# Optimization experiments

Hardware: AMD Instinct MI355X
Metric: run time of the kernel (lower is better)

Reference implementation:

```python
import jax, jax.numpy as jnp
import numpy as np

H, D, VD = 8, 64, 64
QD, KD, VDIM, OUT = 512, 512, 512, 512
N, QS, VS = 16, 512, 512
TEMP = 10.0              # softstair_temp
SCALING = D ** -0.5


def _softstair(x):
    fl = jnp.floor(x)
    return fl + jax.nn.sigmoid(TEMP * (jnp.abs(x - fl) - 0.5))


def setup_inputs() -> dict:
    key = jax.random.key(0)
    ks = jax.random.split(key, 24)
    f = jax.random.normal
    s = 0.03  # xavier-ish scale
    return {
        "Q": f(ks[0], (N, QS, QD), jnp.float32),
        "K": f(ks[1], (N, VS, KD), jnp.float32),
        "V": f(ks[2], (N, VS, VDIM), jnp.float32),
        "past_state": f(ks[3], (N, H, QS, D), jnp.float32),
        "past_attention": jax.random.uniform(ks[4], (N, H, QS, 1), jnp.float32),
        "value_positions": jnp.arange(VS, dtype=jnp.float32),
        "attention_mask": jnp.ones((N, QS, VS), jnp.int32),
        "Wq": f(ks[5], (QD, H * D), jnp.float32) * s,
        "Wk": f(ks[6], (KD, H * D), jnp.float32) * s,
        "Wv": f(ks[7], (VDIM, H * VD), jnp.float32) * s,
        "Wpos": f(ks[8], (QD, H * D), jnp.float32) * s,
        "bpos": f(ks[9], (H * D,), jnp.float32) * s,
        "Wsigma": f(ks[10], (H, D, 1), jnp.float32) * s,
        "Wrho": f(ks[11], (H, D, 3), jnp.float32) * s,
        "mix_w": f(ks[12], (QD, 1), jnp.float32) * s,
        "mix_b": f(ks[13], (1,), jnp.float32) * s,
        "gru_wi": f(ks[14], (D, 3 * D), jnp.float32) * s,
        "gru_wh": f(ks[15], (D, 3 * D), jnp.float32) * s,
        "gru_bi": f(ks[16], (3 * D,), jnp.float32) * s,
        "gru_bh": f(ks[17], (3 * D,), jnp.float32) * s,
        "Wc": f(ks[18], (H * VD, OUT), jnp.float32) * s,
    }


def reference(Q, K, V, past_state, past_attention, value_positions, attention_mask,
              Wq, Wk, Wv, Wpos, bpos, Wsigma, Wrho, mix_w, mix_b,
              gru_wi, gru_wh, gru_bi, gru_bh, Wc):
    n, qS, _ = Q.shape
    vS = K.shape[1]
    mask_f = attention_mask.astype(jnp.float32)          # [N,qS,vS]
    mask_b = attention_mask.astype(bool)[:, None]        # [N,1,qS,vS]
    lengths = jnp.sum(mask_f, axis=-1)                   # [N,qS]
    l_1 = jnp.maximum(1.0, lengths - 1.0)[:, None, :, None]
    step_size = 1.0 / l_1                                # [N,1,qS,1]
    nvp = value_positions[None, None, None, :] * step_size  # [N,1,qS,vS]

    # mix gate
    mix = jax.nn.sigmoid(Q @ mix_w + mix_b)[:, None]     # [N,1,qS,1]

    # projections -> [N,H,S,d]
    Qpos = (Q @ Wpos + bpos).reshape(n, qS, H, D).transpose(0, 2, 1, 3)
    Qh = (Q @ Wq).reshape(n, qS, H, D).transpose(0, 2, 1, 3)
    Kh = (K @ Wk).reshape(n, vS, H, D).transpose(0, 2, 1, 3)
    Vh = (V @ Wv).reshape(n, vS, H, VD).transpose(0, 2, 1, 3)

    # content attention
    content = jnp.einsum('bhqd,bhkd->bhqk', Qh, Kh) * SCALING
    content_attn = jax.nn.softmax(jnp.where(mask_b, content, -jnp.inf), axis=-1)

    # GRUCell update (torch gate order r,z,n) on relu(Qpos) with past_state
    x = jax.nn.relu(Qpos)
    gi = x @ gru_wi + gru_bi
    gh = past_state @ gru_wh + gru_bh
    ir, iz, inn = jnp.split(gi, 3, axis=-1)
    hr, hz, hn = jnp.split(gh, 3, axis=-1)
    r = jax.nn.sigmoid(ir + hr)
    z = jax.nn.sigmoid(iz + hz)
    nn_ = jnp.tanh(inn + r * hn)
    state = (1.0 - z) * nn_ + z * past_state             # [N,H,qS,D]

    # location (Gaussian) attention
    sigma = (jax.nn.relu(jnp.einsum('bhqd,hde->bhqe', state, Wsigma)) + 0.27) \
            / lengths[:, None, :, None]                  # [N,H,qS,1]
    rho = jnp.einsum('bhqd,hde->bhqe', state, Wrho)      # [N,H,qS,3]
    steps = _softstair(rho[..., 0:1])
    attn_gate = jax.nn.sigmoid(rho[..., 1:2])
    bias_gate = jax.nn.sigmoid(rho[..., 2:3])
    mu_ = steps * step_size + attn_gate * past_attention + bias_gate
    # leaky clamp to [0,1]
    mu = jnp.maximum(0.01 * mu_, jnp.minimum(mu_, 1.0 + 0.01 * mu_))
    diff = nvp - mu                                      # [N,H,qS,vS]
    gauss = jnp.exp(-(diff * diff) / (2.0 * sigma * sigma))
    g = gauss * mask_f[:, None]
    pos_attn = g / jnp.sum(g + 1e-20, axis=-1, keepdims=True)

    scores = mix * pos_attn + (1.0 - mix) * content_attn
    attended = jnp.einsum('bhqk,bhkv->bhqv', scores, Vh)
    out = attended.transpose(0, 2, 1, 3).reshape(n, qS, H * VD) @ Wc
    return out
```

## Files before the change

### kernel.cpp

```cpp
#include <hip/hip_runtime.h>


typedef __bf16 bf16;
typedef __bf16 bfx8 __attribute__((ext_vector_type(8)));
typedef float v4f __attribute__((ext_vector_type(4)));

__device__ inline float sigm(float x) { return 1.0f / (1.0f + __expf(-x)); }
__device__ inline float tanh_fast(float x) { return 1.0f - 2.0f / (__expf(2.0f * x) + 1.0f); }

__device__ inline v4f mfma16(bfx8 a, bfx8 b, v4f c) {
    return __builtin_amdgcn_mfma_f32_16x16x32_bf16(a, b, c, 0, 0, 0);
}

__device__ inline void split8(const float* __restrict__ p, bfx8& hi, bfx8& lo) {
    float4 x = *(const float4*)p;
    float4 y = *(const float4*)(p + 4);
    float v[8] = {x.x, x.y, x.z, x.w, y.x, y.y, y.z, y.w};
#pragma unroll
    for (int j = 0; j < 8; ++j) {
        bf16 h = (bf16)v[j];
        hi[j] = h;
        lo[j] = (bf16)(v[j] - (float)h);
    }
}

__device__ inline bfx8 cvt8(const float* __restrict__ p) {
    float4 x = *(const float4*)p;
    float4 y = *(const float4*)(p + 4);
    bfx8 o;
    o[0] = (bf16)x.x; o[1] = (bf16)x.y; o[2] = (bf16)x.z; o[3] = (bf16)x.w;
    o[4] = (bf16)y.x; o[5] = (bf16)y.y; o[6] = (bf16)y.z; o[7] = (bf16)y.w;
    return o;
}

__device__ inline unsigned short bfbits(float v) {
    bf16 h = (bf16)v;
    return __builtin_bit_cast(unsigned short, h);
}
__device__ inline float bffrom(unsigned short u) {
    return (float)__builtin_bit_cast(bf16, u);
}

struct TW { const float* src[5]; bf16* dst[5]; bf16* dstlo[5]; };

__global__ __launch_bounds__(256) void trans_w_kernel(TW a) {
    __shared__ float tile[64][68];
    const float* src = a.src[blockIdx.y];
    bf16* dst = a.dst[blockIdx.y];
    bf16* dlo = a.dstlo[blockIdx.y];
    const int rbase = (blockIdx.x >> 3) * 64, cbase = (blockIdx.x & 7) * 64;
    const int t = threadIdx.x;
    const int r = t >> 2, cc = (t & 3) * 16;
    {
        const float* p = src + (long)(rbase + r) * 512 + cbase + cc;
        *(float4*)(&tile[r][cc]) = *(const float4*)p;
        *(float4*)(&tile[r][cc + 4]) = *(const float4*)(p + 4);
        *(float4*)(&tile[r][cc + 8]) = *(const float4*)(p + 8);
        *(float4*)(&tile[r][cc + 12]) = *(const float4*)(p + 12);
    }
    __syncthreads();
    {
        bfx8 h0, h1, l0, l1;
#pragma unroll
        for (int j = 0; j < 8; ++j) {
            float v0 = tile[cc + j][r];
            float v1 = tile[cc + 8 + j][r];
            bf16 a0 = (bf16)v0, a1 = (bf16)v1;
            h0[j] = a0; l0[j] = (bf16)(v0 - (float)a0);
            h1[j] = a1; l1[j] = (bf16)(v1 - (float)a1);
        }
        bf16* p = dst + (long)(cbase + r) * 512 + rbase + cc;
        *(bfx8*)p = h0;
        *(bfx8*)(p + 8) = h1;
        if (dlo) {
            bf16* pl = dlo + (long)(cbase + r) * 512 + rbase + cc;
            *(bfx8*)pl = l0;
            *(bfx8*)(pl + 8) = l1;
        }
    }
}

__global__ void gru_prep_kernel(const float* __restrict__ gwi, const float* __restrict__ gwh,
                                bf16* ih, bf16* il, bf16* hh, bf16* hl) {
    const float* src = blockIdx.x ? gwh : gwi;
    bf16* dh = blockIdx.x ? hh : ih;
    bf16* dl = blockIdx.x ? hl : il;
    int n = threadIdx.x;
    for (int k = 0; k < 64; ++k) {
        float v = src[k * 192 + n];
        bf16 h = (bf16)v;
        dh[n * 64 + k] = h;
        dl[n * 64 + k] = (bf16)(v - (float)h);
    }
}

struct G3 { const float* A[3]; const bf16* BT[3]; bf16* C[3]; };

__global__ __launch_bounds__(256) void gemm_bt3(G3 g) {
    __shared__ bf16 As[64][72];
    __shared__ bf16 Bs[64][72];

    const int z = blockIdx.z;
    const float* __restrict__ A = g.A[z];
    const bf16* __restrict__ BT = g.BT[z];
    bf16* __restrict__ C = g.C[z];

    const int mbase = blockIdx.x * 64, nbase = blockIdx.y * 64;
    const int t = threadIdx.x;
    const int wave = t >> 6, lane = t & 63;
    const int quad = lane >> 4, c = lane & 15;
    const int wrow = (wave >> 1) * 32, wcol = (wave & 1) * 32;

    const v4f zero4 = {0.f, 0.f, 0.f, 0.f};
    v4f acc[2][2];
    acc[0][0] = zero4; acc[0][1] = zero4; acc[1][0] = zero4; acc[1][1] = zero4;

    const int sr = t >> 2, sch = t & 3;

    for (int k0 = 0; k0 < 512; k0 += 32) {
        bfx8 va = cvt8(A + (long)(mbase + sr) * 512 + k0 + sch * 8);
        bfx8 vb = *(const bfx8*)(BT + (long)(nbase + sr) * 512 + k0 + sch * 8);
        *(bfx8*)(&As[sr][sch * 8]) = va;
        *(bfx8*)(&Bs[sr][sch * 8]) = vb;
        __syncthreads();

        bfx8 a0 = *(const bfx8*)(&As[wrow + c][quad * 8]);
        bfx8 a1 = *(const bfx8*)(&As[wrow + 16 + c][quad * 8]);
        bfx8 b0 = *(const bfx8*)(&Bs[wcol + c][quad * 8]);
        bfx8 b1 = *(const bfx8*)(&Bs[wcol + 16 + c][quad * 8]);
        acc[0][0] = mfma16(a0, b0, acc[0][0]);
        acc[0][1] = mfma16(a0, b1, acc[0][1]);
        acc[1][0] = mfma16(a1, b0, acc[1][0]);
        acc[1][1] = mfma16(a1, b1, acc[1][1]);
        __syncthreads();
    }

    if (z == 2) {
#pragma unroll
        for (int tm = 0; tm < 2; ++tm)
#pragma unroll
            for (int tn = 0; tn < 2; ++tn)
#pragma unroll
                for (int i = 0; i < 4; ++i) {
                    int rl = wrow + tm * 16 + quad * 4 + i;
                    int cl = wcol + tn * 16 + c;
                    As[cl][rl] = (bf16)acc[tm][tn][i];
                }
        __syncthreads();
        bf16* CT = C + ((long)(mbase >> 9)) * 262144 + (long)nbase * 512 + (mbase & 511);
        const int rr = t >> 2, kc = (t & 3) * 16;
        bfx8 o0, o1;
#pragma unroll
        for (int j = 0; j < 8; ++j) { o0[j] = As[rr][kc + j]; o1[j] = As[rr][kc + 8 + j]; }
        *(bfx8*)(CT + (long)rr * 512 + kc) = o0;
        *(bfx8*)(CT + (long)rr * 512 + kc + 8) = o1;
    } else {
#pragma unroll
        for (int tm = 0; tm < 2; ++tm)
#pragma unroll
            for (int tn = 0; tn < 2; ++tn)
#pragma unroll
                for (int i = 0; i < 4; ++i) {
                    int row = mbase + wrow + tm * 16 + quad * 4 + i;
                    int col = nbase + wcol + tn * 16 + c;
                    C[(long)row * 512 + col] = (bf16)acc[tm][tn][i];
                }
    }
}

__global__ __launch_bounds__(256) void gemm_out(
    const bf16* __restrict__ A, const bf16* __restrict__ BT, float* __restrict__ C) {
    __shared__ bf16 As[64][72];
    __shared__ bf16 Bs[64][72];

    const int mbase = blockIdx.x * 64, nbase = blockIdx.y * 64;
    const int t = threadIdx.x;
    const int wave = t >> 6, lane = t & 63;
    const int quad = lane >> 4, c = lane & 15;
    const int wrow = (wave >> 1) * 32, wcol = (wave & 1) * 32;

    const v4f zero4 = {0.f, 0.f, 0.f, 0.f};
    v4f acc[2][2];
    acc[0][0] = zero4; acc[0][1] = zero4; acc[1][0] = zero4; acc[1][1] = zero4;

    const int sr = t >> 2, sch = t & 3;

    for (int k0 = 0; k0 < 512; k0 += 32) {
        bfx8 va = *(const bfx8*)(A + (long)(mbase + sr) * 512 + k0 + sch * 8);
        bfx8 vb = *(const bfx8*)(BT + (long)(nbase + sr) * 512 + k0 + sch * 8);
        *(bfx8*)(&As[sr][sch * 8]) = va;
        *(bfx8*)(&Bs[sr][sch * 8]) = vb;
        __syncthreads();

        bfx8 a0 = *(const bfx8*)(&As[wrow + c][quad * 8]);
        bfx8 a1 = *(const bfx8*)(&As[wrow + 16 + c][quad * 8]);
        bfx8 b0 = *(const bfx8*)(&Bs[wcol + c][quad * 8]);
        bfx8 b1 = *(const bfx8*)(&Bs[wcol + 16 + c][quad * 8]);
        acc[0][0] = mfma16(a0, b0, acc[0][0]);
        acc[0][1] = mfma16(a0, b1, acc[0][1]);
        acc[1][0] = mfma16(a1, b0, acc[1][0]);
        acc[1][1] = mfma16(a1, b1, acc[1][1]);
        __syncthreads();
    }

#pragma unroll
    for (int tm = 0; tm < 2; ++tm)
#pragma unroll
        for (int tn = 0; tn < 2; ++tn)
#pragma unroll
            for (int i = 0; i < 4; ++i) {
                int row = mbase + wrow + tm * 16 + quad * 4 + i;
                int col = nbase + wcol + tn * 16 + c;
                C[(long)row * 512 + col] = acc[tm][tn][i];
            }
}

__global__ __launch_bounds__(256) void gemm_split_hl(
    const float* __restrict__ A, const bf16* __restrict__ BTh,
    const bf16* __restrict__ BTl, const float* __restrict__ bias,
    bf16* __restrict__ Ch, bf16* __restrict__ Cl) {
    __shared__ bf16 Ah[64][72], Al[64][72];
    __shared__ bf16 Bh[64][72], Bl[64][72];

    const int mbase = blockIdx.x * 64, nbase = blockIdx.y * 64;
    const int t = threadIdx.x;
    const int wave = t >> 6, lane = t & 63;
    const int quad = lane >> 4, c = lane & 15;
    const int wrow = (wave >> 1) * 32, wcol = (wave & 1) * 32;

    const v4f zero4 = {0.f, 0.f, 0.f, 0.f};
    v4f acc[2][2];
    acc[0][0] = zero4; acc[0][1] = zero4; acc[1][0] = zero4; acc[1][1] = zero4;

    const int sr = t >> 2, sch = t & 3;

    for (int k0 = 0; k0 < 512; k0 += 32) {
        bfx8 h, l;
        split8(A + (long)(mbase + sr) * 512 + k0 + sch * 8, h, l);
        *(bfx8*)(&Ah[sr][sch * 8]) = h;
        *(bfx8*)(&Al[sr][sch * 8]) = l;
        *(bfx8*)(&Bh[sr][sch * 8]) = *(const bfx8*)(BTh + (long)(nbase + sr) * 512 + k0 + sch * 8);
        *(bfx8*)(&Bl[sr][sch * 8]) = *(const bfx8*)(BTl + (long)(nbase + sr) * 512 + k0 + sch * 8);
        __syncthreads();

        bfx8 ah0 = *(const bfx8*)(&Ah[wrow + c][quad * 8]);
        bfx8 ah1 = *(const bfx8*)(&Ah[wrow + 16 + c][quad * 8]);
        bfx8 al0 = *(const bfx8*)(&Al[wrow + c][quad * 8]);
        bfx8 al1 = *(const bfx8*)(&Al[wrow + 16 + c][quad * 8]);
        bfx8 bh0 = *(const bfx8*)(&Bh[wcol + c][quad * 8]);
        bfx8 bh1 = *(const bfx8*)(&Bh[wcol + 16 + c][quad * 8]);
        bfx8 bl0 = *(const bfx8*)(&Bl[wcol + c][quad * 8]);
        bfx8 bl1 = *(const bfx8*)(&Bl[wcol + 16 + c][quad * 8]);
        acc[0][0] = mfma16(ah0, bh0, acc[0][0]);
        acc[0][0] = mfma16(ah0, bl0, acc[0][0]);
        acc[0][0] = mfma16(al0, bh0, acc[0][0]);
        acc[0][1] = mfma16(ah0, bh1, acc[0][1]);
        acc[0][1] = mfma16(ah0, bl1, acc[0][1]);
        acc[0][1] = mfma16(al0, bh1, acc[0][1]);
        acc[1][0] = mfma16(ah1, bh0, acc[1][0]);
        acc[1][0] = mfma16(ah1, bl0, acc[1][0]);
        acc[1][0] = mfma16(al1, bh0, acc[1][0]);
        acc[1][1] = mfma16(ah1, bh1, acc[1][1]);
        acc[1][1] = mfma16(ah1, bl1, acc[1][1]);
        acc[1][1] = mfma16(al1, bh1, acc[1][1]);
        __syncthreads();
    }

#pragma unroll
    for (int tm = 0; tm < 2; ++tm)
#pragma unroll
        for (int tn = 0; tn < 2; ++tn)
#pragma unroll
            for (int i = 0; i < 4; ++i) {
                int row = mbase + wrow + tm * 16 + quad * 4 + i;
                int col = nbase + wcol + tn * 16 + c;
                float v = fmaxf(acc[tm][tn][i] + bias[col], 0.f);
                bf16 h = (bf16)v;
                Ch[(long)row * 512 + col] = h;
                Cl[(long)row * 512 + col] = (bf16)(v - (float)h);
            }
}

__global__ __launch_bounds__(256) void mix_len_kernel(
    const float* __restrict__ Q, const int* __restrict__ mask,
    const float* __restrict__ mix_w, const float* __restrict__ mix_b,
    float* __restrict__ mixv, float* __restrict__ stepv, float* __restrict__ lenv,
    unsigned* __restrict__ maskbits) {
    int row = blockIdx.x * 4 + (threadIdx.x >> 6);
    int lane = threadIdx.x & 63;
    float dot = 0.f, ms = 0.f;
    unsigned myw = 0;
#pragma unroll
    for (int j = 0; j < 8; ++j) {
        float qv = Q[(long)row * 512 + j * 64 + lane];
        float wv = mix_w[j * 64 + lane];
        dot += qv * wv;
        int mv = mask[(long)row * 512 + j * 64 + lane];
        unsigned long long b = __ballot(mv != 0);
        ms += (float)__popcll(b);
        if ((lane >> 1) == j) myw = (unsigned)(b >> ((lane & 1) * 32));
    }
#pragma unroll
    for (int o = 32; o > 0; o >>= 1) dot += __shfl_xor(dot, o);
    if (lane < 16) maskbits[(long)row * 16 + lane] = myw;
    if (lane == 0) {
        mixv[row] = sigm(dot + mix_b[0]);
        lenv[row] = ms;
        stepv[row] = 1.0f / fmaxf(1.0f, ms - 1.0f);
    }
}

__global__ __launch_bounds__(256) void gru_fused_kernel(
    const bf16* __restrict__ Xh, const bf16* __restrict__ Xl,
    const float* __restrict__ hp,
    const bf16* __restrict__ wih, const bf16* __restrict__ wil,
    const bf16* __restrict__ whh, const bf16* __restrict__ whl,
    const float* __restrict__ gbi, const float* __restrict__ gbh,
    const float* __restrict__ pa, const float* __restrict__ Wsigma,
    const float* __restrict__ Wrho,
    const float* __restrict__ lenv, const float* __restrict__ stepv,
    float* __restrict__ muv, float* __restrict__ sigv) {
    __shared__ bf16 Wh[192][72], Wl[192][72];
    __shared__ float biL[384];

    const int b = blockIdx.x;
    const int qb = b & 7, nh = b >> 3, hd = nh & 7, n = nh >> 3;
    const int t = threadIdx.x;
    const int w = t >> 6, lane = t & 63, quad = lane >> 4, c = lane & 15;
    const int q0 = qb * 64 + w * 16;

    if (t < 192) { biL[t] = gbi[t]; biL[192 + t] = gbh[t]; }
#pragma unroll
    for (int it = 0; it < 6; ++it) {
        int task = it * 256 + t;
        int r = task >> 3, ch = task & 7;
        *(bfx8*)(&Wh[r][ch * 8]) = *(const bfx8*)(wih + r * 64 + ch * 8);
        *(bfx8*)(&Wl[r][ch * 8]) = *(const bfx8*)(wil + r * 64 + ch * 8);
    }
    __syncthreads();

    const v4f zero4 = {0.f, 0.f, 0.f, 0.f};
    v4f gi[12], gh[12];
#pragma unroll
    for (int nt = 0; nt < 12; ++nt) gi[nt] = zero4;
#pragma unroll
    for (int ks = 0; ks < 2; ++ks) {
        long ao = (long)(n * 512 + q0 + c) * 512 + hd * 64 + ks * 32 + quad * 8;
        bfx8 xh = *(const bfx8*)(Xh + ao);
        bfx8 xl = *(const bfx8*)(Xl + ao);
#pragma unroll
        for (int nt = 0; nt < 12; ++nt) {
            bfx8 bh = *(const bfx8*)(&Wh[nt * 16 + c][ks * 32 + quad * 8]);
            bfx8 bl = *(const bfx8*)(&Wl[nt * 16 + c][ks * 32 + quad * 8]);
            gi[nt] = mfma16(xh, bh, gi[nt]);
            gi[nt] = mfma16(xh, bl, gi[nt]);
            gi[nt] = mfma16(xl, bh, gi[nt]);
        }
    }
    __syncthreads();
#pragma unroll
    for (int it = 0; it < 6; ++it) {
        int task = it * 256 + t;
        int r = task >> 3, ch = task & 7;
        *(bfx8*)(&Wh[r][ch * 8]) = *(const bfx8*)(whh + r * 64 + ch * 8);
        *(bfx8*)(&Wl[r][ch * 8]) = *(const bfx8*)(whl + r * 64 + ch * 8);
    }
    __syncthreads();
#pragma unroll
    for (int nt = 0; nt < 12; ++nt) gh[nt] = zero4;
#pragma unroll
    for (int ks = 0; ks < 2; ++ks) {
        bfx8 ah, al;
        split8(hp + (long)(nh * 512 + q0 + c) * 64 + ks * 32 + quad * 8, ah, al);
#pragma unroll
        for (int nt = 0; nt < 12; ++nt) {
            bfx8 bh = *(const bfx8*)(&Wh[nt * 16 + c][ks * 32 + quad * 8]);
            bfx8 bl = *(const bfx8*)(&Wl[nt * 16 + c][ks * 32 + quad * 8]);
            gh[nt] = mfma16(ah, bh, gh[nt]);
            gh[nt] = mfma16(ah, bl, gh[nt]);
            gh[nt] = mfma16(al, bh, gh[nt]);
        }
    }

    float st[4][4];
#pragma unroll
    for (int t4 = 0; t4 < 4; ++t4) {
        float bir = biL[t4 * 16 + c];
        float biz = biL[64 + t4 * 16 + c];
        float bin = biL[128 + t4 * 16 + c];
        float bhr = biL[192 + t4 * 16 + c];
        float bhz = biL[256 + t4 * 16 + c];
        float bhn = biL[320 + t4 * 16 + c];
#pragma unroll
        for (int i = 0; i < 4; ++i) {
            int row = q0 + quad * 4 + i;
            float r = sigm(gi[t4][i] + bir + gh[t4][i] + bhr);
            float z = sigm(gi[t4 + 4][i] + biz + gh[t4 + 4][i] + bhz);
            float nn_ = tanh_fast(gi[t4 + 8][i] + bin + r * (gh[t4 + 8][i] + bhn));
            float hpv = hp[(long)(nh * 512 + row) * 64 + t4 * 16 + c];
            st[t4][i] = (1.0f - z) * nn_ + z * hpv;
        }
    }

    float ws_[4], wr0[4], wr1[4], wr2[4];
#pragma unroll
    for (int t4 = 0; t4 < 4; ++t4) {
        int d = t4 * 16 + c;
        ws_[t4] = Wsigma[hd * 64 + d];
        wr0[t4] = Wrho[(hd * 64 + d) * 3 + 0];
        wr1[t4] = Wrho[(hd * 64 + d) * 3 + 1];
        wr2[t4] = Wrho[(hd * 64 + d) * 3 + 2];
    }
#pragma unroll
    for (int i = 0; i < 4; ++i) {
        float s0 = 0.f, s1 = 0.f, s2 = 0.f, s3 = 0.f;
#pragma unroll
        for (int t4 = 0; t4 < 4; ++t4) {
            float sv = st[t4][i];
            s0 += sv * ws_[t4];
            s1 += sv * wr0[t4];
            s2 += sv * wr1[t4];
            s3 += sv * wr2[t4];
        }
#pragma unroll
        for (int o = 1; o < 16; o <<= 1) {
            s0 += __shfl_xor(s0, o);
            s1 += __shfl_xor(s1, o);
            s2 += __shfl_xor(s2, o);
            s3 += __shfl_xor(s3, o);
        }
        if (c == 0) {
            int row = q0 + quad * 4 + i;
            int idx = nh * 512 + row, rq = n * 512 + row;
            float L = lenv[rq], sp = stepv[rq];
            float sg = (fmaxf(s0, 0.f) + 0.27f) / L;
            float fl = floorf(s1);
            float steps = fl + sigm(10.0f * (fabsf(s1 - fl) - 0.5f));
            float ag = sigm(s2), bg = sigm(s3);
            float mu_ = steps * sp + ag * pa[idx] + bg;
            float mu = fmaxf(0.01f * mu_, fminf(mu_, 1.0f + 0.01f * mu_));
            muv[idx] = mu;
            sigv[idx] = sg;
        }
    }
}

__global__ __launch_bounds__(256) void attn_fused_kernel(
    const bf16* __restrict__ Qh, const bf16* __restrict__ Kh,
    const bf16* __restrict__ VhT, const unsigned* __restrict__ maskbits,
    const float* __restrict__ vpos, const float* __restrict__ mixv,
    const float* __restrict__ stepv, const float* __restrict__ muv,
    const float* __restrict__ sigv, bf16* __restrict__ att) {
    __shared__ bf16 Plds[16][520];
    __shared__ float vps[512];
    __shared__ unsigned mb[16][16];
    __shared__ float rmax[4][16], rsum[4][16], rgsum[4][16];
    __shared__ float rowmu[16], rowsig[16], rowstep[16], rowmix[16];

    const int b = blockIdx.x;
    const int nh = ((b >> 8) << 3) | (b & 7);
    const int qt = (b >> 3) & 31;
    const int hd = nh & 7, n = nh >> 3;
    const int t = threadIdx.x;

    if (t < 16) {
        int q = qt * 16 + t;
        int idx = nh * 512 + q, rq = n * 512 + q;
        rowmu[t] = muv[idx];
        rowsig[t] = sigv[idx];
        rowstep[t] = stepv[rq];
        rowmix[t] = mixv[rq];
    }
    vps[t] = vpos[t];
    vps[256 + t] = vpos[256 + t];
    mb[t >> 4][t & 15] = maskbits[(long)(n * 512 + qt * 16 + (t >> 4)) * 16 + (t & 15)];

    const int wave = t >> 6, lane = t & 63;
    const int quad = lane >> 4, c = lane & 15;
    const int qloc = quad * 4;

    const bf16* qrow = Qh + (long)(n * 512 + qt * 16 + c) * 512 + hd * 64 + quad * 8;
    bfx8 afr0 = *(const bfx8*)qrow;
    bfx8 afr1 = *(const bfx8*)(qrow + 32);

    const v4f zero4 = {0.f, 0.f, 0.f, 0.f};
    v4f acc[8];
#pragma unroll
    for (int i = 0; i < 8; ++i) acc[i] = zero4;

    const bf16* kbase = Kh + (long)(n * 512 + wave * 128 + c) * 512 + hd * 64 + quad * 8;
#pragma unroll
    for (int t8 = 0; t8 < 8; ++t8) {
        bfx8 b0 = *(const bfx8*)(kbase + (long)t8 * 16 * 512);
        bfx8 b1 = *(const bfx8*)(kbase + (long)t8 * 16 * 512 + 32);
        acc[t8] = mfma16(afr0, b0, acc[t8]);
        acc[t8] = mfma16(afr1, b1, acc[t8]);
    }
#pragma unroll
    for (int t8 = 0; t8 < 8; ++t8) acc[t8] = acc[t8] * 0.125f;

    __syncthreads();

    unsigned mbits[4] = {0u, 0u, 0u, 0u};
#pragma unroll
    for (int t8 = 0; t8 < 8; ++t8) {
        int wd = wave * 4 + (t8 >> 1);
        int bit = (t8 & 1) * 16 + c;
#pragma unroll
        for (int i = 0; i < 4; ++i)
            mbits[i] |= ((mb[qloc + i][wd] >> bit) & 1u) << t8;
    }

#pragma unroll
    for (int i = 0; i < 4; ++i) {
        float mx = -3.0e38f;
#pragma unroll
        for (int t8 = 0; t8 < 8; ++t8)
            if ((mbits[i] >> t8) & 1u) mx = fmaxf(mx, acc[t8][i]);
        mx = fmaxf(mx, __shfl_xor(mx, 1));
        mx = fmaxf(mx, __shfl_xor(mx, 2));
        mx = fmaxf(mx, __shfl_xor(mx, 4));
        mx = fmaxf(mx, __shfl_xor(mx, 8));
        if (c == 0) rmax[wave][qloc + i] = mx;
    }
    __syncthreads();

    float gmx[4], inv2s[4];
#pragma unroll
    for (int i = 0; i < 4; ++i) {
        gmx[i] = fmaxf(fmaxf(rmax[0][qloc + i], rmax[1][qloc + i]),
                       fmaxf(rmax[2][qloc + i], rmax[3][qloc + i]));
        float sg = rowsig[qloc + i];
        inv2s[i] = 0.5f / (sg * sg);
    }

    float psum[4] = {0.f, 0.f, 0.f, 0.f};
    float gsum[4] = {0.f, 0.f, 0.f, 0.f};
    unsigned pg[8][4];
#pragma unroll
    for (int t8 = 0; t8 < 8; ++t8) {
        int k = wave * 128 + t8 * 16 + c;
        float vp = vps[k];
#pragma unroll
        for (int i = 0; i < 4; ++i) {
            int on = (mbits[i] >> t8) & 1;
            float pv = on ? __expf(acc[t8][i] - gmx[i]) : 0.f;
            float d = vp * rowstep[qloc + i] - rowmu[qloc + i];
            float gv = on ? __expf(-(d * d) * inv2s[i]) : 0.f;
            psum[i] += pv;
            gsum[i] += gv;
            pg[t8][i] = ((unsigned)bfbits(gv) << 16) | (unsigned)bfbits(pv);
        }
    }
#pragma unroll
    for (int i = 0; i < 4; ++i) {
#pragma unroll
        for (int o = 1; o < 16; o <<= 1) {
            psum[i] += __shfl_xor(psum[i], o);
            gsum[i] += __shfl_xor(gsum[i], o);
        }
        if (c == 0) {
            rsum[wave][qloc + i] = psum[i];
            rgsum[wave][qloc + i] = gsum[i];
        }
    }
    __syncthreads();

    float ac[4], bc[4];
#pragma unroll
    for (int i = 0; i < 4; ++i) {
        float Sp = rsum[0][qloc + i] + rsum[1][qloc + i] + rsum[2][qloc + i] + rsum[3][qloc + i];
        float Sg = rgsum[0][qloc + i] + rgsum[1][qloc + i] + rgsum[2][qloc + i] +
                   rgsum[3][qloc + i] + 512.0f * 1e-20f;
        float m_ = rowmix[qloc + i];
        ac[i] = (1.0f - m_) / Sp;
        bc[i] = m_ / Sg;
    }

#pragma unroll
    for (int t8 = 0; t8 < 8; ++t8) {
        int k = wave * 128 + t8 * 16 + c;
#pragma unroll
        for (int i = 0; i < 4; ++i) {
            float pv = bffrom((unsigned short)(pg[t8][i] & 0xffffu));
            float gv = bffrom((unsigned short)(pg[t8][i] >> 16));
            Plds[qloc + i][k] = (bf16)(pv * ac[i] + gv * bc[i]);
        }
    }
    __syncthreads();

    v4f accO = zero4;
    const bf16* vrow = VhT + (long)(n * 512 + hd * 64 + wave * 16 + c) * 512 + quad * 8;
#pragma unroll
    for (int ks = 0; ks < 16; ++ks) {
        bfx8 af = *(const bfx8*)(&Plds[c][ks * 32 + quad * 8]);
        bfx8 bf_ = *(const bfx8*)(vrow + ks * 32);
        accO = mfma16(af, bf_, accO);
    }

#pragma unroll
    for (int i = 0; i < 4; ++i) {
        att[(long)(n * 512 + qt * 16 + quad * 4 + i) * 512 + hd * 64 + wave * 16 + c] =
            (bf16)accO[i];
    }
}

extern "C" void kernel_launch(void* const* d_in, const int* in_sizes, int n_in,
                              void* d_out, int out_size, void* d_ws, size_t ws_size,
                              hipStream_t stream) {
    (void)in_sizes; (void)n_in; (void)out_size; (void)ws_size;

    const float* Q = (const float*)d_in[0];
    const float* K = (const float*)d_in[1];
    const float* V = (const float*)d_in[2];
    const float* past_state = (const float*)d_in[3];
    const float* past_att = (const float*)d_in[4];
    const float* vpos = (const float*)d_in[5];
    const int* mask = (const int*)d_in[6];
    const float* Wq = (const float*)d_in[7];
    const float* Wk = (const float*)d_in[8];
    const float* Wv = (const float*)d_in[9];
    const float* Wpos = (const float*)d_in[10];
    const float* bpos = (const float*)d_in[11];
    const float* Wsigma = (const float*)d_in[12];
    const float* Wrho = (const float*)d_in[13];
    const float* mix_w = (const float*)d_in[14];
    const float* mix_b = (const float*)d_in[15];
    const float* gwi = (const float*)d_in[16];
    const float* gwh = (const float*)d_in[17];
    const float* gbi = (const float*)d_in[18];
    const float* gbh = (const float*)d_in[19];
    const float* Wc = (const float*)d_in[20];
    float* out = (float*)d_out;

    char* p = (char*)d_ws;
    const size_t SZB = 8192UL * 512 * 2;
    const size_t SZW = 512UL * 512 * 2;
    bf16* WqT = (bf16*)p;   p += SZW;
    bf16* WkT = (bf16*)p;   p += SZW;
    bf16* WvT = (bf16*)p;   p += SZW;
    bf16* WpT = (bf16*)p;   p += SZW;
    bf16* WpTl = (bf16*)p;  p += SZW;
    bf16* WcT = (bf16*)p;   p += SZW;
    bf16* wih = (bf16*)p;   p += 24576;
    bf16* wil = (bf16*)p;   p += 24576;
    bf16* whh = (bf16*)p;   p += 24576;
    bf16* whl = (bf16*)p;   p += 24576;
    bf16* Qh = (bf16*)p;    p += SZB;
    bf16* Kh = (bf16*)p;    p += SZB;
    bf16* VhT = (bf16*)p;   p += SZB;
    bf16* Xh = (bf16*)p;
    bf16* att = Xh;         p += SZB;
    bf16* Xl = (bf16*)p;    p += SZB;
    unsigned* maskbits = (unsigned*)p;   p += 8192UL * 16 * 4;
    float* mixv = (float*)p;  p += 32768;
    float* stepv = (float*)p; p += 32768;
    float* lenv = (float*)p;  p += 32768;
    float* muv = (float*)p;   p += 262144;
    float* sigv = (float*)p;  p += 262144;

    dim3 blk(256);
    dim3 gProj(128, 8, 1);

    TW tw;
    tw.src[0] = Wq; tw.src[1] = Wk; tw.src[2] = Wv; tw.src[3] = Wpos; tw.src[4] = Wc;
    tw.dst[0] = WqT; tw.dst[1] = WkT; tw.dst[2] = WvT; tw.dst[3] = WpT; tw.dst[4] = WcT;
    tw.dstlo[0] = nullptr; tw.dstlo[1] = nullptr; tw.dstlo[2] = nullptr;
    tw.dstlo[3] = WpTl; tw.dstlo[4] = nullptr;
    trans_w_kernel<<<dim3(64, 5), blk, 0, stream>>>(tw);

    gru_prep_kernel<<<dim3(2), dim3(192), 0, stream>>>(gwi, gwh, wih, wil, whh, whl);

    G3 g;
    g.A[0] = Q; g.A[1] = K; g.A[2] = V;
    g.BT[0] = WqT; g.BT[1] = WkT; g.BT[2] = WvT;
    g.C[0] = Qh; g.C[1] = Kh; g.C[2] = VhT;
    gemm_bt3<<<dim3(128, 8, 3), blk, 0, stream>>>(g);

    gemm_split_hl<<<gProj, blk, 0, stream>>>(Q, WpT, WpTl, bpos, Xh, Xl);

    mix_len_kernel<<<dim3(2048), blk, 0, stream>>>(Q, mask, mix_w, mix_b, mixv, stepv, lenv, maskbits);

    gru_fused_kernel<<<dim3(1024), blk, 0, stream>>>(
        Xh, Xl, past_state, wih, wil, whh, whl, gbi, gbh, past_att, Wsigma, Wrho,
        lenv, stepv, muv, sigv);

    attn_fused_kernel<<<dim3(4096), blk, 0, stream>>>(
        Qh, Kh, VhT, maskbits, vpos, mixv, stepv, muv, sigv, att);

    gemm_out<<<gProj, blk, 0, stream>>>(att, WcT, out);
}
```

Before: 361.3 us.

## Drop softmax max pass, split P/G matmuls, defer normalization to output

The attention kernel now skips the row-max reduction and its barrier and exponentiates scaled scores directly. This relies on the scores being small enough not to overflow. It writes unnormalized content and positional weights to two LDS tiles and runs two MFMA accumulations against V. Both normalizations and the mix are applied to the final accumulators, which removes one barrier and the per-element rescale pass, at the cost of doubling the P·V MFMA work and LDS reads. Per-row parameters, mask bits and value positions are now read straight from global memory instead of being staged in shared memory.

```diff
diff --git a/kernel.cpp b/kernel.cpp
--- a/kernel.cpp
+++ b/kernel.cpp
@@ -31,14 +31,6 @@
     o[0] = (bf16)x.x; o[1] = (bf16)x.y; o[2] = (bf16)x.z; o[3] = (bf16)x.w;
     o[4] = (bf16)y.x; o[5] = (bf16)y.y; o[6] = (bf16)y.z; o[7] = (bf16)y.w;
     return o;
-}
-
-__device__ inline unsigned short bfbits(float v) {
-    bf16 h = (bf16)v;
-    return __builtin_bit_cast(unsigned short, h);
-}
-__device__ inline float bffrom(unsigned short u) {
-    return (float)__builtin_bit_cast(bf16, u);
 }
 
 struct TW { const float* src[5]; bf16* dst[5]; bf16* dstlo[5]; };
@@ -451,30 +443,15 @@
     const float* __restrict__ vpos, const float* __restrict__ mixv,
     const float* __restrict__ stepv, const float* __restrict__ muv,
     const float* __restrict__ sigv, bf16* __restrict__ att) {
-    __shared__ bf16 Plds[16][520];
-    __shared__ float vps[512];
-    __shared__ unsigned mb[16][16];
-    __shared__ float rmax[4][16], rsum[4][16], rgsum[4][16];
-    __shared__ float rowmu[16], rowsig[16], rowstep[16], rowmix[16];
+    __shared__ bf16 Pp[16][520];
+    __shared__ bf16 Pg[16][520];
+    __shared__ float rsum[4][16], rgsum[4][16];
 
     const int b = blockIdx.x;
     const int nh = ((b >> 8) << 3) | (b & 7);
     const int qt = (b >> 3) & 31;
     const int hd = nh & 7, n = nh >> 3;
     const int t = threadIdx.x;
-
-    if (t < 16) {
-        int q = qt * 16 + t;
-        int idx = nh * 512 + q, rq = n * 512 + q;
-        rowmu[t] = muv[idx];
-        rowsig[t] = sigv[idx];
-        rowstep[t] = stepv[rq];
-        rowmix[t] = mixv[rq];
-    }
-    vps[t] = vpos[t];
-    vps[256 + t] = vpos[256 + t];
-    mb[t >> 4][t & 15] = maskbits[(long)(n * 512 + qt * 16 + (t >> 4)) * 16 + (t & 15)];
-
     const int wave = t >> 6, lane = t & 63;
     const int quad = lane >> 4, c = lane & 15;
     const int qloc = quad * 4;
@@ -496,60 +473,52 @@
         acc[t8] = mfma16(afr0, b0, acc[t8]);
         acc[t8] = mfma16(afr1, b1, acc[t8]);
     }
-#pragma unroll
-    for (int t8 = 0; t8 < 8; ++t8) acc[t8] = acc[t8] * 0.125f;
-
-    __syncthreads();
-
-    unsigned mbits[4] = {0u, 0u, 0u, 0u};
-#pragma unroll
-    for (int t8 = 0; t8 < 8; ++t8) {
-        int wd = wave * 4 + (t8 >> 1);
-        int bit = (t8 & 1) * 16 + c;
-#pragma unroll
-        for (int i = 0; i < 4; ++i)
-            mbits[i] |= ((mb[qloc + i][wd] >> bit) & 1u) << t8;
-    }
-
+
+    float mu_[4], i2s[4], stp[4];
 #pragma unroll
     for (int i = 0; i < 4; ++i) {
-        float mx = -3.0e38f;
-#pragma unroll
-        for (int t8 = 0; t8 < 8; ++t8)
-            if ((mbits[i] >> t8) & 1u) mx = fmaxf(mx, acc[t8][i]);
-        mx = fmaxf(mx, __shfl_xor(mx, 1));
-        mx = fmaxf(mx, __shfl_xor(mx, 2));
-        mx = fmaxf(mx, __shfl_xor(mx, 4));
-        mx = fmaxf(mx, __shfl_xor(mx, 8));
-        if (c == 0) rmax[wave][qloc + i] = mx;
-    }
-    __syncthreads();
-
-    float gmx[4], inv2s[4];
-#pragma unroll
-    for (int i = 0; i < 4; ++i) {
-        gmx[i] = fmaxf(fmaxf(rmax[0][qloc + i], rmax[1][qloc + i]),
-                       fmaxf(rmax[2][qloc + i], rmax[3][qloc + i]));
-        float sg = rowsig[qloc + i];
-        inv2s[i] = 0.5f / (sg * sg);
-    }
+        int q = qt * 16 + qloc + i;
+        int idx = nh * 512 + q, rq = n * 512 + q;
+        mu_[i] = muv[idx];
+        float sg = sigv[idx];
+        i2s[i] = 0.5f / (sg * sg);
+        stp[i] = stepv[rq];
+    }
+
+    unsigned mbits[4];
+    {
+        const unsigned* mrow = maskbits + ((long)(n * 512 + qt * 16) << 4) + wave * 4;
+#pragma unroll
+        for (int i = 0; i < 4; ++i) {
+            const unsigned* mr = mrow + ((qloc + i) << 4);
+            unsigned w0 = mr[0], w1 = mr[1], w2 = mr[2], w3 = mr[3];
+            mbits[i] = ((w0 >> c) & 1u) | (((w0 >> (16 + c)) & 1u) << 1) |
+                       (((w1 >> c) & 1u) << 2) | (((w1 >> (16 + c)) & 1u) << 3) |
+                       (((w2 >> c) & 1u) << 4) | (((w2 >> (16 + c)) & 1u) << 5) |
+                       (((w3 >> c) & 1u) << 6) | (((w3 >> (16 + c)) & 1u) << 7);
+        }
+    }
+
+    float vp[8];
+#pragma unroll
+    for (int t8 = 0; t8 < 8; ++t8) vp[t8] = vpos[wave * 128 + t8 * 16 + c];
 
     float psum[4] = {0.f, 0.f, 0.f, 0.f};
     float gsum[4] = {0.f, 0.f, 0.f, 0.f};
-    unsigned pg[8][4];
-#pragma unroll
-    for (int t8 = 0; t8 < 8; ++t8) {
-        int k = wave * 128 + t8 * 16 + c;
-        float vp = vps[k];
-#pragma unroll
-        for (int i = 0; i < 4; ++i) {
+#pragma unroll
+    for (int i = 0; i < 4; ++i) {
+        float m = mu_[i], s = stp[i], c2 = i2s[i];
+#pragma unroll
+        for (int t8 = 0; t8 < 8; ++t8) {
             int on = (mbits[i] >> t8) & 1;
-            float pv = on ? __expf(acc[t8][i] - gmx[i]) : 0.f;
-            float d = vp * rowstep[qloc + i] - rowmu[qloc + i];
-            float gv = on ? __expf(-(d * d) * inv2s[i]) : 0.f;
+            float pv = on ? __expf(acc[t8][i] * 0.125f) : 0.f;
+            float d = vp[t8] * s - m;
+            float gv = on ? __expf(-(d * d) * c2) : 0.f;
             psum[i] += pv;
             gsum[i] += gv;
-            pg[t8][i] = ((unsigned)bfbits(gv) << 16) | (unsigned)bfbits(pv);
+            int k = wave * 128 + t8 * 16 + c;
+            Pp[qloc + i][k] = (bf16)pv;
+            Pg[qloc + i][k] = (bf16)gv;
         }
     }
 #pragma unroll
@@ -564,6 +533,7 @@
             rgsum[wave][qloc + i] = gsum[i];
         }
     }
+
     __syncthreads();
 
     float ac[4], bc[4];
@@ -572,36 +542,26 @@
         float Sp = rsum[0][qloc + i] + rsum[1][qloc + i] + rsum[2][qloc + i] + rsum[3][qloc + i];
         float Sg = rgsum[0][qloc + i] + rgsum[1][qloc + i] + rgsum[2][qloc + i] +
                    rgsum[3][qloc + i] + 512.0f * 1e-20f;
-        float m_ = rowmix[qloc + i];
+        float m_ = mixv[n * 512 + qt * 16 + qloc + i];
         ac[i] = (1.0f - m_) / Sp;
         bc[i] = m_ / Sg;
     }
 
-#pragma unroll
-    for (int t8 = 0; t8 < 8; ++t8) {
-        int k = wave * 128 + t8 * 16 + c;
-#pragma unroll
-        for (int i = 0; i < 4; ++i) {
-            float pv = bffrom((unsigned short)(pg[t8][i] & 0xffffu));
-            float gv = bffrom((unsigned short)(pg[t8][i] >> 16));
-            Plds[qloc + i][k] = (bf16)(pv * ac[i] + gv * bc[i]);
-        }
-    }
-    __syncthreads();
-
-    v4f accO = zero4;
+    v4f accP = zero4, accG = zero4;
     const bf16* vrow = VhT + (long)(n * 512 + hd * 64 + wave * 16 + c) * 512 + quad * 8;
 #pragma unroll
     for (int ks = 0; ks < 16; ++ks) {
-        bfx8 af = *(const bfx8*)(&Plds[c][ks * 32 + quad * 8]);
         bfx8 bf_ = *(const bfx8*)(vrow + ks * 32);
-        accO = mfma16(af, bf_, accO);
+        bfx8 ap = *(const bfx8*)(&Pp[c][ks * 32 + quad * 8]);
+        bfx8 ag = *(const bfx8*)(&Pg[c][ks * 32 + quad * 8]);
+        accP = mfma16(ap, bf_, accP);
+        accG = mfma16(ag, bf_, accG);
     }
 
 #pragma unroll
     for (int i = 0; i < 4; ++i) {
         att[(long)(n * 512 + qt * 16 + quad * 4 + i) * 512 + hd * 64 + wave * 16 + c] =
-            (bf16)accO[i];
+            (bf16)(ac[i] * accP[i] + bc[i] * accG[i]);
     }
 }
 
```

New measurement: 347.4 us. 1.04x faster.
